# Performance work log

Measured on AMD Instinct MI355X. Metric: run time of the kernel, lower is better.

## Reference

```python
import jax, jax.numpy as jnp
import numpy as np

K = 5            # kernel_size per pseudo-dim
N = 51200        # nodes
E = 819200       # edges (avg degree 16)
B = 64           # graphs in batch

# 2^dim corner offsets for degree-1 (linear) open B-spline in dim=2
_BITS = jnp.array([[0, 0], [0, 1], [1, 0], [1, 1]], dtype=jnp.int32)  # [4,2]

def spline_basis(pseudo):
    # pseudo: [E,2] in [0,1]. Returns basis [E,4], weight indices [E,4].
    v = pseudo * (K - 1)
    lo = jnp.clip(jnp.floor(v).astype(jnp.int32), 0, K - 2)   # [E,2]
    frac = v - lo.astype(pseudo.dtype)                        # [E,2]
    idx = lo[:, None, :] + _BITS[None]                        # [E,4,2]
    w = jnp.where(_BITS[None] == 1, frac[:, None, :], 1.0 - frac[:, None, :])
    basis = w.prod(-1)                                        # [E,4]
    widx = idx[..., 0] * K + idx[..., 1]                      # [E,4] in [0,25)
    return basis, widx

def spline_conv(x, src, dst, basis, widx, W, root, bias):
    # x:[N,Fin], W:[25,Fin,Fout], root:[Fin,Fout], bias:[Fout]
    n = x.shape[0]
    Z = jnp.einsum('ni,kio->nko', x, W)          # [N,25,Fout] per-node per-kernel transforms
    Zg = Z[src[:, None], widx]                   # [E,4,Fout] irregular gather
    msg = jnp.einsum('es,eso->eo', basis, Zg)    # [E,Fout]
    agg = jax.ops.segment_sum(msg, dst, num_segments=n)
    deg = jax.ops.segment_sum(jnp.ones_like(msg[:, 0]), dst, num_segments=n)
    agg = agg / jnp.maximum(deg, 1.0)[:, None]   # mean aggregation
    return agg + x @ root + bias

def setup_inputs():
    key = jax.random.key(0)
    ks = jax.random.split(key, 12)
    x = jax.random.normal(ks[0], (N, 7), jnp.float32)
    edge_index = jax.random.randint(ks[1], (2, E), 0, N, dtype=jnp.int32)
    pseudo = jax.random.uniform(ks[2], (E, 2), jnp.float32)
    slices = jnp.arange(B + 1, dtype=jnp.int32) * (N // B)   # graph boundaries
    W1 = jax.random.normal(ks[3], (K * K, 7, 32), jnp.float32) * 0.2
    root1 = jax.random.normal(ks[4], (7, 32), jnp.float32) * 0.2
    b1 = jnp.zeros((32,), jnp.float32)
    W2 = jax.random.normal(ks[5], (K * K, 32, 64), jnp.float32) * 0.1
    root2 = jax.random.normal(ks[6], (32, 64), jnp.float32) * 0.1
    b2 = jnp.zeros((64,), jnp.float32)
    fc_w = jax.random.normal(ks[7], (64, 30), jnp.float32) * 0.1
    fc_b = jnp.zeros((30,), jnp.float32)
    return {"x": x, "edge_index": edge_index, "pseudo": pseudo, "slices": slices,
            "W1": W1, "root1": root1, "b1": b1, "W2": W2, "root2": root2,
            "b2": b2, "fc_w": fc_w, "fc_b": fc_b}

def reference(x, edge_index, pseudo, slices, W1, root1, b1, W2, root2, b2, fc_w, fc_b):
    src, dst = edge_index[0], edge_index[1]
    basis, widx = spline_basis(pseudo)
    h = jax.nn.elu(spline_conv(x, src, dst, basis, widx, W1, root1, b1))
    h = jax.nn.elu(spline_conv(h, src, dst, basis, widx, W2, root2, b2))
    # batch_average: mean of node features per graph (slices = boundaries)
    gid = jnp.clip(jnp.searchsorted(slices, jnp.arange(N), side='right') - 1, 0, B - 1)
    sums = jax.ops.segment_sum(h, gid, num_segments=B)
    counts = (slices[1:] - slices[:-1]).astype(h.dtype)
    g = sums / jnp.maximum(counts, 1.0)[:, None]             # [B,64]
    # dropout is identity in eval mode
    logits = g @ fc_w + fc_b
    return jax.nn.log_softmax(logits, axis=-1)
```

## Files before the change

### kernel.cpp

```cpp
#include <hip/hip_runtime.h>
#include <hip/hip_fp16.h>
#include <math.h>

#define N_NODES 51200
#define N_EDGES 819200
#define NB 64
#define CAP 64

typedef _Float16 half8 __attribute__((ext_vector_type(8)));
typedef __attribute__((ext_vector_type(4))) float float4v;

__device__ __forceinline__ float eluf(float x) {
  return x > 0.f ? x : expm1f(x);
}

__device__ __forceinline__ void dec2(int w0, int w1, int c, float& basf, int& Kc) {
  int K = w0 >> 16;
  float f0 = __half2float(__ushort_as_half((unsigned short)(w1 & 0xFFFF)));
  float f1 = __half2float(__ushort_as_half((unsigned short)(((unsigned)w1) >> 16)));
  float b0 = (c & 2) ? f0 : 1.f - f0;
  float bv = (c & 1) ? f1 : 1.f - f1;
  Kc = K + (c >> 1) * 5 + (c & 1);
  basf = b0 * bv;
}

__device__ __forceinline__ void rmw16(unsigned* Tr, int Kc, int q, float bf, int4 hv) {
  __half2 bas = __float2half2_rn(bf);
  __half2* tp = (__half2*)&Tr[Kc * 16 + q * 4];
  const __half2* h = (const __half2*)&hv;
  __half2 t0 = tp[0], t1 = tp[1], t2 = tp[2], t3 = tp[3];
  tp[0] = __hfma2(bas, h[0], t0);
  tp[1] = __hfma2(bas, h[1], t1);
  tp[2] = __hfma2(bas, h[2], t2);
  tp[3] = __hfma2(bas, h[3], t3);
}

__global__ __launch_bounds__(256) void prep(const float* __restrict__ x,
                                            const float* __restrict__ W1,
                                            const float* __restrict__ root1,
                                            const float* __restrict__ W2,
                                            const float* __restrict__ root2,
                                            __half* __restrict__ xh,
                                            __half* __restrict__ W1T,
                                            __half* __restrict__ W2T,
                                            float* __restrict__ gbuf) {
  int b = blockIdx.x, tid = threadIdx.x;
  if (b < 1600) {
    int idx = b * 256 + tid;
    int n = idx >> 3, j = idx & 7;
    xh[idx] = __float2half((j < 7) ? x[n * 7 + j] : 0.f);
  } else if (b < 1628) {
    int idx = (b - 1600) * 256 + tid;
    int o = idx / 224, k = idx - o * 224;
    float v = 0.f;
    if (k < 200) {
      int cell = k >> 3, f = k & 7;
      if (f < 7) v = W1[(cell * 7 + f) * 32 + o];
    } else if (k < 207) {
      v = root1[(k - 200) * 32 + o];
    }
    W1T[idx] = __float2half(v);
  } else if (b < 1836) {
    int idx = (b - 1628) * 256 + tid;
    int o = idx / 832, k = idx - o * 832;
    float v = (k < 800) ? W2[k * 64 + o] : root2[(k - 800) * 64 + o];
    W2T[idx] = __float2half(v);
  } else {
    int idx = (b - 1836) * 256 + tid;
    gbuf[idx] = 0.f;
  }
}

__global__ __launch_bounds__(256) void scatter_eid(const int* __restrict__ ei,
                                                   const float* __restrict__ pseudo,
                                                   int* __restrict__ cnt,
                                                   int2* __restrict__ bucket) {
  int base = blockIdx.x * 2048 + threadIdx.x;
#pragma unroll
  for (int u = 0; u < 8; u++) {
    int e = base + u * 256;
    int src = ei[e], dst = ei[N_EDGES + e];
    float v0 = pseudo[2 * e] * 4.f;
    float v1 = pseudo[2 * e + 1] * 4.f;
    int lo0 = min(max((int)floorf(v0), 0), 3);
    int lo1 = min(max((int)floorf(v1), 0), 3);
    float f0 = v0 - (float)lo0, f1 = v1 - (float)lo1;
    int K = lo0 * 5 + lo1;
    unsigned short u0 = __half_as_ushort(__float2half(f0));
    unsigned short u1 = __half_as_ushort(__float2half(f1));
    int w0 = src | (K << 16);
    int w1 = (int)((unsigned)u0 | ((unsigned)u1 << 16));
    int slot = atomicAdd(&cnt[dst], 1);
    if (slot < CAP) bucket[(size_t)dst * CAP + slot] = make_int2(w0, w1);
  }
}

#define L1N 16
__global__ __launch_bounds__(256) void fused_l1(const int2* __restrict__ bucket,
                                                const int* __restrict__ cnt,
                                                const unsigned* __restrict__ xh,
                                                const __half* __restrict__ W1T,
                                                const float* __restrict__ b1,
                                                unsigned short* __restrict__ h1h) {
  __shared__ unsigned T[L1N * 112];
  __shared__ float invdeg_s[L1N];
  int tid = threadIdx.x;
  int n0 = blockIdx.x * L1N;
  for (int idx = tid; idx < L1N * 112; idx += 256) T[idx] = 0u;
  if (tid < L1N) invdeg_s[tid] = 1.f / fmaxf((float)cnt[n0 + tid], 1.f);
  __syncthreads();
  if (tid < L1N * 4) {
    int row = tid >> 2, p = tid & 3;
    int n = n0 + row;
    float dgc = fmaxf((float)cnt[n], 1.f);
    unsigned xv = xh[n * 4 + p];
    __half2 h = __hmul2(*(const __half2*)&xv, __float2half2_rn(dgc));
    T[row * 112 + 100 + p] = *(unsigned*)&h;
  }
  int wv = tid >> 6, l = tid & 63;
  int slot = l >> 4, c = (l >> 2) & 3, p = l & 3;
  int nn = wv * 4 + slot;
  int n = n0 + nn;
  int dg = min(cnt[n], CAP);
  int dmax = dg;
  dmax = max(dmax, __shfl_xor(dmax, 16));
  dmax = max(dmax, __shfl_xor(dmax, 32));
  const int2* bk = bucket + (size_t)n * CAP;
  unsigned* Tr = &T[nn * 112];
  int4 ra0 = *(const int4*)(bk + 0);
  int4 rb0 = *(const int4*)(bk + 2);
  int4 ra1 = *(const int4*)(bk + 4);
  int4 rb1 = *(const int4*)(bk + 6);
  unsigned xv0 = xh[(ra0.x & 0xFFFF) * 4 + p];
  unsigned xv1 = xh[(ra0.z & 0xFFFF) * 4 + p];
  unsigned xv2 = xh[(rb0.x & 0xFFFF) * 4 + p];
  unsigned xv3 = xh[(rb0.z & 0xFFFF) * 4 + p];
  for (int j = 0; j < dmax; j += 4) {
    int jp = min(j + 8, CAP - 4);
    int4 ra2 = *(const int4*)(bk + jp);
    int4 rb2 = *(const int4*)(bk + jp + 2);
    unsigned nx0 = xh[(ra1.x & 0xFFFF) * 4 + p];
    unsigned nx1 = xh[(ra1.z & 0xFFFF) * 4 + p];
    unsigned nx2 = xh[(rb1.x & 0xFFFF) * 4 + p];
    unsigned nx3 = xh[(rb1.z & 0xFFFF) * 4 + p];
    bool a0 = j < dg, a1 = j + 1 < dg, a2 = j + 2 < dg, a3 = j + 3 < dg;
    float bf; int Kc;
    if (a0) { dec2(ra0.x, ra0.y, c, bf, Kc);
      __half2* tp = (__half2*)&Tr[Kc * 4 + p];
      *tp = __hfma2(__float2half2_rn(bf), *(const __half2*)&xv0, *tp); }
    if (a1) { dec2(ra0.z, ra0.w, c, bf, Kc);
      __half2* tp = (__half2*)&Tr[Kc * 4 + p];
      *tp = __hfma2(__float2half2_rn(bf), *(const __half2*)&xv1, *tp); }
    if (a2) { dec2(rb0.x, rb0.y, c, bf, Kc);
      __half2* tp = (__half2*)&Tr[Kc * 4 + p];
      *tp = __hfma2(__float2half2_rn(bf), *(const __half2*)&xv2, *tp); }
    if (a3) { dec2(rb0.z, rb0.w, c, bf, Kc);
      __half2* tp = (__half2*)&Tr[Kc * 4 + p];
      *tp = __hfma2(__float2half2_rn(bf), *(const __half2*)&xv3, *tp); }
    ra0 = ra1; rb0 = rb1; ra1 = ra2; rb1 = rb2;
    xv0 = nx0; xv1 = nx1; xv2 = nx2; xv3 = nx3;
  }
  __syncthreads();
  if (wv < 2) {
    int m = l & 15, quad = l >> 4;
    const char* abase = (const char*)T + m * 448 + quad * 16;
    const __half* bbase = W1T + (wv * 16 + m) * 224 + quad * 8;
    float4v acc = {0.f, 0.f, 0.f, 0.f};
#pragma unroll
    for (int it = 0; it < 7; it++) {
      half8 af = *(const half8*)(abase + it * 64);
      half8 bf = *(const half8*)(bbase + it * 32);
      acc = __builtin_amdgcn_mfma_f32_16x16x32_f16(af, bf, acc, 0, 0, 0);
    }
    int feat = wv * 16 + m;
    float bb = b1[feat];
#pragma unroll
    for (int r = 0; r < 4; r++) {
      int row = quad * 4 + r;
      float v = eluf(acc[r] * invdeg_s[row] + bb);
      h1h[(size_t)(n0 + row) * 32 + feat] = __half_as_ushort(__float2half(v));
    }
  }
}

#define L2N 16
__global__ __launch_bounds__(256) void fused_l2(const int2* __restrict__ bucket,
                                                const int* __restrict__ cnt,
                                                const unsigned* __restrict__ h1hu,
                                                const __half* __restrict__ W2T,
                                                const float* __restrict__ b2,
                                                float* __restrict__ gbuf) {
  __shared__ unsigned T[L2N * 420];
  __shared__ float invdeg_s[L2N];
  int tid = threadIdx.x;
  int n0 = blockIdx.x * L2N;
  for (int idx = tid; idx < L2N * 420; idx += 256) T[idx] = 0u;
  if (tid < L2N) invdeg_s[tid] = 1.f / fmaxf((float)cnt[n0 + tid], 1.f);
  __syncthreads();
  {
    int row = tid >> 4, p = tid & 15;
    int n = n0 + row;
    float dgc = fmaxf((float)cnt[n], 1.f);
    unsigned hv = h1hu[(size_t)n * 16 + p];
    __half2 h = __hmul2(*(const __half2*)&hv, __float2half2_rn(dgc));
    T[row * 420 + 400 + p] = *(unsigned*)&h;
  }
  int wv = tid >> 6, l = tid & 63;
  int slot = l >> 4, c = (l >> 2) & 3, q = l & 3;
  int nn = wv * 4 + slot;
  int n = n0 + nn;
  int dg = min(cnt[n], CAP);
  int dmax = dg;
  dmax = max(dmax, __shfl_xor(dmax, 16));
  dmax = max(dmax, __shfl_xor(dmax, 32));
  const int2* bk = bucket + (size_t)n * CAP;
  unsigned* Tr = &T[nn * 420];
  const unsigned* h1q = h1hu + q * 4;
  int4 ra0 = *(const int4*)(bk + 0);
  int4 rb0 = *(const int4*)(bk + 2);
  int4 ra1 = *(const int4*)(bk + 4);
  int4 rb1 = *(const int4*)(bk + 6);
  int4 hv0 = *(const int4*)(h1q + (size_t)(ra0.x & 0xFFFF) * 16);
  int4 hv1 = *(const int4*)(h1q + (size_t)(ra0.z & 0xFFFF) * 16);
  int4 hv2 = *(const int4*)(h1q + (size_t)(rb0.x & 0xFFFF) * 16);
  int4 hv3 = *(const int4*)(h1q + (size_t)(rb0.z & 0xFFFF) * 16);
  for (int j = 0; j < dmax; j += 4) {
    int jp = min(j + 8, CAP - 4);
    int4 ra2 = *(const int4*)(bk + jp);
    int4 rb2 = *(const int4*)(bk + jp + 2);
    int4 nh0 = *(const int4*)(h1q + (size_t)(ra1.x & 0xFFFF) * 16);
    int4 nh1 = *(const int4*)(h1q + (size_t)(ra1.z & 0xFFFF) * 16);
    int4 nh2 = *(const int4*)(h1q + (size_t)(rb1.x & 0xFFFF) * 16);
    int4 nh3 = *(const int4*)(h1q + (size_t)(rb1.z & 0xFFFF) * 16);
    bool a0 = j < dg, a1 = j + 1 < dg, a2 = j + 2 < dg, a3 = j + 3 < dg;
    float bf; int Kc;
    if (a0) { dec2(ra0.x, ra0.y, c, bf, Kc); rmw16(Tr, Kc, q, bf, hv0); }
    if (a1) { dec2(ra0.z, ra0.w, c, bf, Kc); rmw16(Tr, Kc, q, bf, hv1); }
    if (a2) { dec2(rb0.x, rb0.y, c, bf, Kc); rmw16(Tr, Kc, q, bf, hv2); }
    if (a3) { dec2(rb0.z, rb0.w, c, bf, Kc); rmw16(Tr, Kc, q, bf, hv3); }
    ra0 = ra1; rb0 = rb1; ra1 = ra2; rb1 = rb2;
    hv0 = nh0; hv1 = nh1; hv2 = nh2; hv3 = nh3;
  }
  __syncthreads();
  int m = l & 15, quad = l >> 4;
  const char* abase = (const char*)T + m * 1680 + quad * 16;
  const __half* bbase = W2T + (size_t)(wv * 16 + m) * 832 + quad * 8;
  float4v acc = {0.f, 0.f, 0.f, 0.f};
  for (int it = 0; it < 26; it++) {
    half8 af = *(const half8*)(abase + it * 64);
    half8 bf = *(const half8*)(bbase + it * 32);
    acc = __builtin_amdgcn_mfma_f32_16x16x32_f16(af, bf, acc, 0, 0, 0);
  }
  int feat = wv * 16 + m;
  float bb = b2[feat];
  float psum = 0.f;
#pragma unroll
  for (int r = 0; r < 4; r++) {
    int node = quad * 4 + r;
    psum += eluf(acc[r] * invdeg_s[node] + bb);
  }
  psum += __shfl_xor(psum, 16);
  psum += __shfl_xor(psum, 32);
  if (l < 16) {
    int g = n0 / 800;
    atomicAdd(&gbuf[g * 64 + feat], psum);
  }
}

__global__ __launch_bounds__(64) void fc_ls(const float* __restrict__ gbuf,
                                            const int* __restrict__ slices,
                                            const float* __restrict__ fcw,
                                            const float* __restrict__ fcb,
                                            float* __restrict__ out) {
  int g = blockIdx.x;
  int l = threadIdx.x;
  float scale = 1.f / fmaxf((float)(slices[g + 1] - slices[g]), 1.f);
  float logit = -INFINITY;
  if (l < 30) {
    float acc = fcb[l];
    for (int i = 0; i < 64; i++) acc += gbuf[g * 64 + i] * scale * fcw[i * 30 + l];
    logit = acc;
  }
  float m = logit;
  for (int off = 16; off; off >>= 1) m = fmaxf(m, __shfl_xor(m, off, 32));
  float e = (l < 30) ? expf(logit - m) : 0.f;
  for (int off = 16; off; off >>= 1) e += __shfl_xor(e, off, 32);
  if (l < 30) out[g * 30 + l] = logit - m - logf(e);
}

extern "C" void kernel_launch(void* const* d_in, const int* in_sizes, int n_in,
                              void* d_out, int out_size, void* d_ws, size_t ws_size,
                              hipStream_t stream) {
  const float* x      = (const float*)d_in[0];
  const int*   ei     = (const int*)d_in[1];
  const float* pseudo = (const float*)d_in[2];
  const int*   slices = (const int*)d_in[3];
  const float* W1     = (const float*)d_in[4];
  const float* root1  = (const float*)d_in[5];
  const float* b1     = (const float*)d_in[6];
  const float* W2     = (const float*)d_in[7];
  const float* root2  = (const float*)d_in[8];
  const float* b2     = (const float*)d_in[9];
  const float* fcw    = (const float*)d_in[10];
  const float* fcb    = (const float*)d_in[11];
  float* out = (float*)d_out;

  char* ws = (char*)d_ws;
  int*      cnt    = (int*)ws;
  int2*     bucket = (int2*)(cnt + N_NODES);
  unsigned* h1h    = (unsigned*)(bucket + (size_t)N_NODES * CAP);
  float*    gbuf   = (float*)(h1h + (size_t)N_NODES * 16);
  unsigned* xh     = (unsigned*)(gbuf + 64 * 64);
  __half*   W1T    = (__half*)(xh + (size_t)N_NODES * 4);
  __half*   W2T    = W1T + 32 * 224;

  hipMemsetAsync(cnt, 0, N_NODES * sizeof(int), stream);

  prep<<<1852, 256, 0, stream>>>(x, W1, root1, W2, root2,
                                 (__half*)xh, W1T, W2T, gbuf);
  scatter_eid<<<N_EDGES / 2048, 256, 0, stream>>>(ei, pseudo, cnt, bucket);
  fused_l1<<<N_NODES / L1N, 256, 0, stream>>>(bucket, cnt, xh, W1T, b1,
                                              (unsigned short*)h1h);
  fused_l2<<<N_NODES / L2N, 256, 0, stream>>>(bucket, cnt, h1h, W2T, b2, gbuf);
  fc_ls<<<NB, 64, 0, stream>>>(gbuf, slices, fcw, fcb, out);
}
```

Baseline: 212.5 us.

## Replace LDS half2 scatter-accumulate in layer-2 aggregation with MFMA over edge chunks

The layer-2 per-node basis-weighted aggregation used to do read-modify-write half2 FMAs into a shared table. It now builds, per 16-edge chunk, a sparse basis matrix A (edges x 32 cells) and a gathered feature matrix B (edges x 32 feats) in LDS and accumulates them with a 32x32x16 MFMA, flushing to the table once a node is done. This removes the serialized LDS read-modify-write traffic and keeps the accumulation in fp32. The cost is per-chunk LDS staging, scalar element reads to form the fragments, and padding work for partially filled chunks, all without explicit wave barriers around the staging.

```diff
diff --git a/kernel.cpp b/kernel.cpp
--- a/kernel.cpp
+++ b/kernel.cpp
@@ -9,6 +9,7 @@
 
 typedef _Float16 half8 __attribute__((ext_vector_type(8)));
 typedef __attribute__((ext_vector_type(4))) float float4v;
+typedef __attribute__((ext_vector_type(16))) float float16v;
 
 __device__ __forceinline__ float eluf(float x) {
   return x > 0.f ? x : expm1f(x);
@@ -22,17 +23,6 @@
   float bv = (c & 1) ? f1 : 1.f - f1;
   Kc = K + (c >> 1) * 5 + (c & 1);
   basf = b0 * bv;
-}
-
-__device__ __forceinline__ void rmw16(unsigned* Tr, int Kc, int q, float bf, int4 hv) {
-  __half2 bas = __float2half2_rn(bf);
-  __half2* tp = (__half2*)&Tr[Kc * 16 + q * 4];
-  const __half2* h = (const __half2*)&hv;
-  __half2 t0 = tp[0], t1 = tp[1], t2 = tp[2], t3 = tp[3];
-  tp[0] = __hfma2(bas, h[0], t0);
-  tp[1] = __hfma2(bas, h[1], t1);
-  tp[2] = __hfma2(bas, h[2], t2);
-  tp[3] = __hfma2(bas, h[3], t3);
 }
 
 __global__ __launch_bounds__(256) void prep(const float* __restrict__ x,
@@ -190,66 +180,95 @@
                                                 const __half* __restrict__ W2T,
                                                 const float* __restrict__ b2,
                                                 float* __restrict__ gbuf) {
-  __shared__ unsigned T[L2N * 420];
+  __shared__ unsigned T16[L2N * 420];
+  __shared__ __half AB[4][2][512];
   __shared__ float invdeg_s[L2N];
   int tid = threadIdx.x;
   int n0 = blockIdx.x * L2N;
-  for (int idx = tid; idx < L2N * 420; idx += 256) T[idx] = 0u;
   if (tid < L2N) invdeg_s[tid] = 1.f / fmaxf((float)cnt[n0 + tid], 1.f);
-  __syncthreads();
+  if (tid < L2N * 4) T16[(tid >> 2) * 420 + 416 + (tid & 3)] = 0u;
   {
     int row = tid >> 4, p = tid & 15;
     int n = n0 + row;
     float dgc = fmaxf((float)cnt[n], 1.f);
     unsigned hv = h1hu[(size_t)n * 16 + p];
     __half2 h = __hmul2(*(const __half2*)&hv, __float2half2_rn(dgc));
-    T[row * 420 + 400 + p] = *(unsigned*)&h;
+    T16[row * 420 + 400 + p] = *(unsigned*)&h;
   }
   int wv = tid >> 6, l = tid & 63;
-  int slot = l >> 4, c = (l >> 2) & 3, q = l & 3;
-  int nn = wv * 4 + slot;
-  int n = n0 + nn;
-  int dg = min(cnt[n], CAP);
-  int dmax = dg;
-  dmax = max(dmax, __shfl_xor(dmax, 16));
-  dmax = max(dmax, __shfl_xor(dmax, 32));
-  const int2* bk = bucket + (size_t)n * CAP;
-  unsigned* Tr = &T[nn * 420];
-  const unsigned* h1q = h1hu + q * 4;
-  int4 ra0 = *(const int4*)(bk + 0);
-  int4 rb0 = *(const int4*)(bk + 2);
-  int4 ra1 = *(const int4*)(bk + 4);
-  int4 rb1 = *(const int4*)(bk + 6);
-  int4 hv0 = *(const int4*)(h1q + (size_t)(ra0.x & 0xFFFF) * 16);
-  int4 hv1 = *(const int4*)(h1q + (size_t)(ra0.z & 0xFFFF) * 16);
-  int4 hv2 = *(const int4*)(h1q + (size_t)(rb0.x & 0xFFFF) * 16);
-  int4 hv3 = *(const int4*)(h1q + (size_t)(rb0.z & 0xFFFF) * 16);
-  for (int j = 0; j < dmax; j += 4) {
-    int jp = min(j + 8, CAP - 4);
-    int4 ra2 = *(const int4*)(bk + jp);
-    int4 rb2 = *(const int4*)(bk + jp + 2);
-    int4 nh0 = *(const int4*)(h1q + (size_t)(ra1.x & 0xFFFF) * 16);
-    int4 nh1 = *(const int4*)(h1q + (size_t)(ra1.z & 0xFFFF) * 16);
-    int4 nh2 = *(const int4*)(h1q + (size_t)(rb1.x & 0xFFFF) * 16);
-    int4 nh3 = *(const int4*)(h1q + (size_t)(rb1.z & 0xFFFF) * 16);
-    bool a0 = j < dg, a1 = j + 1 < dg, a2 = j + 2 < dg, a3 = j + 3 < dg;
-    float bf; int Kc;
-    if (a0) { dec2(ra0.x, ra0.y, c, bf, Kc); rmw16(Tr, Kc, q, bf, hv0); }
-    if (a1) { dec2(ra0.z, ra0.w, c, bf, Kc); rmw16(Tr, Kc, q, bf, hv1); }
-    if (a2) { dec2(rb0.x, rb0.y, c, bf, Kc); rmw16(Tr, Kc, q, bf, hv2); }
-    if (a3) { dec2(rb0.z, rb0.w, c, bf, Kc); rmw16(Tr, Kc, q, bf, hv3); }
-    ra0 = ra1; rb0 = rb1; ra1 = ra2; rb1 = rb2;
-    hv0 = nh0; hv1 = nh1; hv2 = nh2; hv3 = nh3;
+  _Float16* Ast = (_Float16*)AB[wv][0];
+  _Float16* Bst = (_Float16*)AB[wv][1];
+  int eL = l >> 2, cL = l & 3;
+  int col = l & 31, kg = l >> 5;
+  int b0c = cL >> 1, b1c = cL & 1;
+  int nb = n0 + wv * 4;
+  int dg0 = min(cnt[nb + 0], CAP), dg1 = min(cnt[nb + 1], CAP);
+  int dg2 = min(cnt[nb + 2], CAP), dg3 = min(cnt[nb + 3], CAP);
+  int nc0 = max(1, (dg0 + 15) >> 4), nc1 = max(1, (dg1 + 15) >> 4);
+  int nc2 = max(1, (dg2 + 15) >> 4), nc3 = max(1, (dg3 + 15) >> 4);
+  int Q = nc0 + nc1 + nc2 + nc3;
+  unsigned dgpack = (unsigned)dg0 | ((unsigned)dg1 << 7) |
+                    ((unsigned)dg2 << 14) | ((unsigned)dg3 << 21);
+  unsigned ncpack = (unsigned)nc0 | ((unsigned)nc1 << 4) |
+                    ((unsigned)nc2 << 8) | ((unsigned)nc3 << 12);
+  const int2* bkb = bucket + (size_t)nb * CAP;
+#define NCH(s) ((int)((ncpack >> ((s) * 4)) & 15))
+#define DGD(s) ((int)((dgpack >> ((s) * 7)) & 127))
+#define ADV(S, T) do { if ((T) + 1 < NCH(S)) (T)++; \
+                       else if ((S) < 3) { (S)++; (T) = 0; } } while (0)
+  int s0 = 0, t0 = 0, s1 = 0, t1 = 0, s2 = 0, t2 = 0;
+  ADV(s1, t1);
+  ADV(s2, t2); ADV(s2, t2);
+  int2 rec0 = bkb[s0 * CAP + t0 * 16 + eL];
+  int2 rec1 = bkb[s1 * CAP + t1 * 16 + eL];
+  int src0i = ((t0 * 16 + eL) < DGD(s0)) ? (rec0.x & 0xFFFF) : 0;
+  int4 Breg0 = *(const int4*)(h1hu + (size_t)src0i * 16 + cL * 4);
+  float16v acc = {};
+  for (int q = 0; q < Q; q++) {
+    int2 rec2 = bkb[s2 * CAP + t2 * 16 + eL];
+    int src1i = ((t1 * 16 + eL) < DGD(s1)) ? (rec1.x & 0xFFFF) : 0;
+    int4 Breg1 = *(const int4*)(h1hu + (size_t)src1i * 16 + cL * 4);
+    bool ein = (t0 * 16 + eL) < DGD(s0);
+    int K = rec0.x >> 16;
+    float f0 = __half2float(__ushort_as_half((unsigned short)(rec0.y & 0xFFFF)));
+    float f1 = __half2float(__ushort_as_half((unsigned short)(((unsigned)rec0.y) >> 16)));
+    float w = (b0c ? f0 : 1.f - f0) * (b1c ? f1 : 1.f - f1);
+    int cell = K + b0c * 5 + b1c;
+    *(int4*)((char*)Ast + l * 16) = make_int4(0, 0, 0, 0);
+    if (ein) Ast[eL * 32 + cell] = (_Float16)w;
+    *(int4*)((char*)Bst + l * 16) = Breg0;
+    half8 af, bf;
+#pragma unroll
+    for (int i = 0; i < 8; i++) {
+      af[i] = Ast[(kg * 8 + i) * 32 + col];
+      bf[i] = Bst[(kg * 8 + i) * 32 + col];
+    }
+    acc = __builtin_amdgcn_mfma_f32_32x32x16_f16(af, bf, acc, 0, 0, 0);
+    if (t0 == NCH(s0) - 1) {
+      __half* Trow = (__half*)&T16[(wv * 4 + s0) * 420];
+#pragma unroll
+      for (int r = 0; r < 16; r++) {
+        int crow = (r & 3) + 8 * (r >> 2) + 4 * kg;
+        if (crow < 25) Trow[crow * 32 + col] = __float2half(acc[r]);
+      }
+      acc = (float16v){};
+      if (s0 < 3) { s0++; t0 = 0; }
+    } else {
+      t0++;
+    }
+    rec0 = rec1; rec1 = rec2; Breg0 = Breg1;
+    ADV(s1, t1);
+    ADV(s2, t2);
   }
   __syncthreads();
   int m = l & 15, quad = l >> 4;
-  const char* abase = (const char*)T + m * 1680 + quad * 16;
+  const char* abase = (const char*)T16 + m * 1680 + quad * 16;
   const __half* bbase = W2T + (size_t)(wv * 16 + m) * 832 + quad * 8;
-  float4v acc = {0.f, 0.f, 0.f, 0.f};
+  float4v acc2 = {0.f, 0.f, 0.f, 0.f};
   for (int it = 0; it < 26; it++) {
-    half8 af = *(const half8*)(abase + it * 64);
-    half8 bf = *(const half8*)(bbase + it * 32);
-    acc = __builtin_amdgcn_mfma_f32_16x16x32_f16(af, bf, acc, 0, 0, 0);
+    half8 a2 = *(const half8*)(abase + it * 64);
+    half8 b2f = *(const half8*)(bbase + it * 32);
+    acc2 = __builtin_amdgcn_mfma_f32_16x16x32_f16(a2, b2f, acc2, 0, 0, 0);
   }
   int feat = wv * 16 + m;
   float bb = b2[feat];
@@ -257,7 +276,7 @@
 #pragma unroll
   for (int r = 0; r < 4; r++) {
     int node = quad * 4 + r;
-    psum += eluf(acc[r] * invdeg_s[node] + bb);
+    psum += eluf(acc2[r] * invdeg_s[node] + bb);
   }
   psum += __shfl_xor(psum, 16);
   psum += __shfl_xor(psum, 32);
```

Result: no change. 215.8 us (+1.6%).

## Sort nodes by degree within each graph to balance per-wave edge loops

Applied to the files above, without the earlier changes.

Adds a build_perm kernel that counting-sorts nodes by in-degree inside each 800-node graph segment. The fused layer kernels then process nodes in that permuted order, so the four nodes sharing a wave have similar degree and the loop bound dmax wastes fewer idle iterations. Keeping the permutation inside each graph preserves the per-graph pooling in layer 2. The cost is an extra kernel launch and scattered node-indexed reads and writes through perm, which reduce locality for cnt, x and h1 accesses.

```diff
diff --git a/kernel.cpp b/kernel.cpp
--- a/kernel.cpp
+++ b/kernel.cpp
@@ -95,23 +95,54 @@
   }
 }
 
+__global__ __launch_bounds__(256) void build_perm(const int* __restrict__ cnt,
+                                                  int* __restrict__ perm) {
+  __shared__ int hist[65];
+  __shared__ int base_s[65];
+  int g = blockIdx.x, tid = threadIdx.x;
+  int n0 = g * 800;
+  if (tid < 65) hist[tid] = 0;
+  __syncthreads();
+  for (int i = tid; i < 800; i += 256) {
+    int d = min(cnt[n0 + i], 64);
+    atomicAdd(&hist[d], 1);
+  }
+  __syncthreads();
+  if (tid == 0) {
+    int s = 0;
+    for (int b = 0; b < 65; b++) { base_s[b] = s; s += hist[b]; }
+  }
+  __syncthreads();
+  for (int i = tid; i < 800; i += 256) {
+    int d = min(cnt[n0 + i], 64);
+    int pos = atomicAdd(&base_s[d], 1);
+    perm[n0 + pos] = n0 + i;
+  }
+}
+
 #define L1N 16
 __global__ __launch_bounds__(256) void fused_l1(const int2* __restrict__ bucket,
                                                 const int* __restrict__ cnt,
+                                                const int* __restrict__ perm,
                                                 const unsigned* __restrict__ xh,
                                                 const __half* __restrict__ W1T,
                                                 const float* __restrict__ b1,
                                                 unsigned short* __restrict__ h1h) {
   __shared__ unsigned T[L1N * 112];
   __shared__ float invdeg_s[L1N];
+  __shared__ int pn_s[L1N];
   int tid = threadIdx.x;
   int n0 = blockIdx.x * L1N;
   for (int idx = tid; idx < L1N * 112; idx += 256) T[idx] = 0u;
-  if (tid < L1N) invdeg_s[tid] = 1.f / fmaxf((float)cnt[n0 + tid], 1.f);
+  if (tid < L1N) {
+    int pn = perm[n0 + tid];
+    pn_s[tid] = pn;
+    invdeg_s[tid] = 1.f / fmaxf((float)cnt[pn], 1.f);
+  }
   __syncthreads();
   if (tid < L1N * 4) {
     int row = tid >> 2, p = tid & 3;
-    int n = n0 + row;
+    int n = pn_s[row];
     float dgc = fmaxf((float)cnt[n], 1.f);
     unsigned xv = xh[n * 4 + p];
     __half2 h = __hmul2(*(const __half2*)&xv, __float2half2_rn(dgc));
@@ -120,7 +151,7 @@
   int wv = tid >> 6, l = tid & 63;
   int slot = l >> 4, c = (l >> 2) & 3, p = l & 3;
   int nn = wv * 4 + slot;
-  int n = n0 + nn;
+  int n = pn_s[nn];
   int dg = min(cnt[n], CAP);
   int dmax = dg;
   dmax = max(dmax, __shfl_xor(dmax, 16));
@@ -178,7 +209,7 @@
     for (int r = 0; r < 4; r++) {
       int row = quad * 4 + r;
       float v = eluf(acc[r] * invdeg_s[row] + bb);
-      h1h[(size_t)(n0 + row) * 32 + feat] = __half_as_ushort(__float2half(v));
+      h1h[(size_t)pn_s[row] * 32 + feat] = __half_as_ushort(__float2half(v));
     }
   }
 }
@@ -186,35 +217,41 @@
 #define L2N 16
 __global__ __launch_bounds__(256) void fused_l2(const int2* __restrict__ bucket,
                                                 const int* __restrict__ cnt,
+                                                const int* __restrict__ perm,
                                                 const unsigned* __restrict__ h1hu,
                                                 const __half* __restrict__ W2T,
                                                 const float* __restrict__ b2,
                                                 float* __restrict__ gbuf) {
-  __shared__ unsigned T[L2N * 420];
+  __shared__ unsigned T16[L2N * 420];
   __shared__ float invdeg_s[L2N];
+  __shared__ int pn_s[L2N];
   int tid = threadIdx.x;
   int n0 = blockIdx.x * L2N;
-  for (int idx = tid; idx < L2N * 420; idx += 256) T[idx] = 0u;
-  if (tid < L2N) invdeg_s[tid] = 1.f / fmaxf((float)cnt[n0 + tid], 1.f);
+  for (int idx = tid; idx < L2N * 420; idx += 256) T16[idx] = 0u;
+  if (tid < L2N) {
+    int pn = perm[n0 + tid];
+    pn_s[tid] = pn;
+    invdeg_s[tid] = 1.f / fmaxf((float)cnt[pn], 1.f);
+  }
   __syncthreads();
   {
     int row = tid >> 4, p = tid & 15;
-    int n = n0 + row;
+    int n = pn_s[row];
     float dgc = fmaxf((float)cnt[n], 1.f);
     unsigned hv = h1hu[(size_t)n * 16 + p];
     __half2 h = __hmul2(*(const __half2*)&hv, __float2half2_rn(dgc));
-    T[row * 420 + 400 + p] = *(unsigned*)&h;
+    T16[row * 420 + 400 + p] = *(unsigned*)&h;
   }
   int wv = tid >> 6, l = tid & 63;
   int slot = l >> 4, c = (l >> 2) & 3, q = l & 3;
   int nn = wv * 4 + slot;
-  int n = n0 + nn;
+  int n = pn_s[nn];
   int dg = min(cnt[n], CAP);
   int dmax = dg;
   dmax = max(dmax, __shfl_xor(dmax, 16));
   dmax = max(dmax, __shfl_xor(dmax, 32));
   const int2* bk = bucket + (size_t)n * CAP;
-  unsigned* Tr = &T[nn * 420];
+  unsigned* Tr = &T16[nn * 420];
   const unsigned* h1q = h1hu + q * 4;
   int4 ra0 = *(const int4*)(bk + 0);
   int4 rb0 = *(const int4*)(bk + 2);
@@ -243,7 +280,7 @@
   }
   __syncthreads();
   int m = l & 15, quad = l >> 4;
-  const char* abase = (const char*)T + m * 1680 + quad * 16;
+  const char* abase = (const char*)T16 + m * 1680 + quad * 16;
   const __half* bbase = W2T + (size_t)(wv * 16 + m) * 832 + quad * 8;
   float4v acc = {0.f, 0.f, 0.f, 0.f};
   for (int it = 0; it < 26; it++) {
@@ -313,14 +350,17 @@
   unsigned* xh     = (unsigned*)(gbuf + 64 * 64);
   __half*   W1T    = (__half*)(xh + (size_t)N_NODES * 4);
   __half*   W2T    = W1T + 32 * 224;
+  int*      perm   = (int*)(W2T + 64 * 832);
 
   hipMemsetAsync(cnt, 0, N_NODES * sizeof(int), stream);
 
   prep<<<1852, 256, 0, stream>>>(x, W1, root1, W2, root2,
                                  (__half*)xh, W1T, W2T, gbuf);
   scatter_eid<<<N_EDGES / 2048, 256, 0, stream>>>(ei, pseudo, cnt, bucket);
-  fused_l1<<<N_NODES / L1N, 256, 0, stream>>>(bucket, cnt, xh, W1T, b1,
+  build_perm<<<NB, 256, 0, stream>>>(cnt, perm);
+  fused_l1<<<N_NODES / L1N, 256, 0, stream>>>(bucket, cnt, perm, xh, W1T, b1,
                                               (unsigned short*)h1h);
-  fused_l2<<<N_NODES / L2N, 256, 0, stream>>>(bucket, cnt, h1h, W2T, b2, gbuf);
+  fused_l2<<<N_NODES / L2N, 256, 0, stream>>>(bucket, cnt, perm, h1h, W2T, b2,
+                                              gbuf);
   fc_ls<<<NB, 64, 0, stream>>>(gbuf, slices, fcw, fcb, out);
 }
```

New measurement: 211.1 us. No clear change (-0.7%).
